# Kernel tuning notes

Hardware: AMD Instinct MI355X
Metric: run time of the kernel (lower is better)

## Reference

```python
import jax, jax.numpy as jnp
import numpy as np

B, S, D, H = 2, 2048, 1024, 16
DH = D // H
MASK_FACTOR = -10000.0
EPS = 1e-6


def setup_inputs() -> dict:
    key = jax.random.key(0)
    ks = jax.random.split(key, 12)
    sc = 1.0 / np.sqrt(D)
    inp = {
        'query': jax.random.normal(ks[0], (B, S, D), jnp.float32),
        'key':   jax.random.normal(ks[1], (B, S, D), jnp.float32),
        'value': jax.random.normal(ks[2], (B, S, D), jnp.float32),
        # mask: 1.0 = masked position (causal), shape (B, 1, Sq, Sk)
        'mask': jnp.broadcast_to(
            (1.0 - jnp.tril(jnp.ones((S, S), jnp.float32)))[None, None], (B, 1, S, S)
        ),
        'wq_w': jax.random.normal(ks[3], (D, D), jnp.float32) * sc,
        'wq_b': jnp.zeros((D,), jnp.float32),
        'wk_w': jax.random.normal(ks[4], (D, D), jnp.float32) * sc,
        'wk_b': jnp.zeros((D,), jnp.float32),
        'wv_w': jax.random.normal(ks[5], (D, D), jnp.float32) * sc,
        'wv_b': jnp.zeros((D,), jnp.float32),
        'wo_w': jax.random.normal(ks[6], (D, D), jnp.float32) * sc,
        'wo_b': jnp.zeros((D,), jnp.float32),
        'ln_g': jnp.ones((D,), jnp.float32),
        'ln_b': jnp.zeros((D,), jnp.float32),
    }
    return inp


def _split_heads(x):
    # (B, S, D) -> (B, H, S, DH)
    b, s, _ = x.shape
    return x.reshape(b, s, H, DH).transpose(0, 2, 1, 3)


def _layer_norm(x, g, b):
    mu = jnp.mean(x, axis=-1, keepdims=True)
    var = jnp.mean(jnp.square(x - mu), axis=-1, keepdims=True)
    return (x - mu) * jax.lax.rsqrt(var + EPS) * g + b


def reference(query, key, value, mask, wq_w, wq_b, wk_w, wk_b, wv_w, wv_b,
              wo_w, wo_b, ln_g, ln_b):
    q = _split_heads(query @ wq_w + wq_b)
    k = _split_heads(key @ wk_w + wk_b)
    v = _split_heads(value @ wv_w + wv_b)

    logits = jnp.einsum('bhqd,bhkd->bhqk', q, k) / jnp.sqrt(jnp.float32(DH))
    logits = logits * (1.0 - mask) + mask * MASK_FACTOR
    attn = jax.nn.softmax(logits, axis=-1)  # (B, H, Sq, Sk)

    ctx = jnp.einsum('bhqk,bhkd->bhqd', attn, v)
    ctx = ctx.transpose(0, 2, 1, 3).reshape(query.shape[0], -1, D)

    out = ctx @ wo_w + wo_b
    out = out + query  # residual
    out = _layer_norm(out, ln_g, ln_b)
    return out, attn
```

## Files before the change

### kernel.cpp

```cpp
#include <hip/hip_runtime.h>

#define B_ 2
#define S_ 2048
#define D_ 1024
#define H_ 16
#define DH_ 64
#define EPS_ 1e-6f

typedef short bf16x8 __attribute__((ext_vector_type(8)));
typedef float f32x4  __attribute__((ext_vector_type(4)));

__device__ __forceinline__ ushort f2bf(float x) {
    uint u = __float_as_uint(x);
    return (ushort)((u + 0x7fffu + ((u >> 16) & 1u)) >> 16);
}
__device__ __forceinline__ float bf2f(ushort h) {
    return __uint_as_float(((uint)h) << 16);
}
__device__ __forceinline__ void split_bf(float x, ushort& hi, ushort& lo) {
    hi = f2bf(x);
    lo = f2bf(x - bf2f(hi));
}

__global__ __launch_bounds__(256) void prep_weights_kernel(
    const float* __restrict__ w0, const float* __restrict__ w1,
    const float* __restrict__ w2, const float* __restrict__ w3,
    ushort* __restrict__ Wth, ushort* __restrict__ Wtl)
{
    const int wi = blockIdx.z;
    const float* W = (wi == 0) ? w0 : (wi == 1) ? w1 : (wi == 2) ? w2 : w3;
    ushort* th = Wth + (size_t)wi * D_ * D_;
    ushort* tl = Wtl + (size_t)wi * D_ * D_;
    const int k0 = blockIdx.x * 32, n0 = blockIdx.y * 32;
    const int tid = threadIdx.x;
    __shared__ float t[32][33];
#pragma unroll
    for (int l = 0; l < 4; ++l) {
        int idx = tid + l * 256;
        int kk = idx >> 5, nn = idx & 31;
        t[kk][nn] = W[(size_t)(k0 + kk) * D_ + n0 + nn];
    }
    __syncthreads();
#pragma unroll
    for (int l = 0; l < 4; ++l) {
        int idx = tid + l * 256;
        int nn = idx >> 5, kk = idx & 31;
        ushort h, lo;
        split_bf(t[kk][nn], h, lo);
        th[(size_t)(n0 + nn) * D_ + k0 + kk] = h;
        tl[(size_t)(n0 + nn) * D_ + k0 + kk] = lo;
    }
}

template <int MODE>
__device__ __forceinline__ void gemm_mfma_body(
    const float* __restrict__ A, const ushort* __restrict__ Bh,
    const ushort* __restrict__ Bl, const float* __restrict__ bias,
    const float* __restrict__ residual, float* __restrict__ Cf,
    ushort* __restrict__ Ch, ushort* __restrict__ Cl,
    int M, int N, int K, int bx, int by)
{
    __shared__ ushort Ah[128][40];
    __shared__ ushort Al[128][40];

    const int tid = threadIdx.x;
    const int lane = tid & 63, w = tid >> 6;
    const int l15 = lane & 15, l4 = lane >> 4;
    const int row0 = by * 128, col0 = bx * 128;
    const int wm = (w >> 1) * 64, wn = (w & 1) * 64;

    const f32x4 zf = {0.f, 0.f, 0.f, 0.f};
    f32x4 acc[4][4];
#pragma unroll
    for (int i = 0; i < 4; ++i)
#pragma unroll
        for (int j = 0; j < 4; ++j) acc[i][j] = zf;

    for (int k0 = 0; k0 < K; k0 += 32) {
#pragma unroll
        for (int l = 0; l < 4; ++l) {
            int idx = tid + l * 256;
            int r = idx >> 3, c4 = (idx & 7) * 4;
            const float4 a = *(const float4*)&A[(size_t)(row0 + r) * K + k0 + c4];
            ushort h0, h1, h2, h3, q0, q1, q2, q3;
            split_bf(a.x, h0, q0); split_bf(a.y, h1, q1);
            split_bf(a.z, h2, q2); split_bf(a.w, h3, q3);
            *(ushort4*)&Ah[r][c4] = make_ushort4(h0, h1, h2, h3);
            *(ushort4*)&Al[r][c4] = make_ushort4(q0, q1, q2, q3);
        }
        bf16x8 bh_[4], bl_[4];
#pragma unroll
        for (int j = 0; j < 4; ++j) {
            const size_t bo = (size_t)(col0 + wn + j * 16 + l15) * K + k0 + l4 * 8;
            bh_[j] = *(const bf16x8*)&Bh[bo];
            bl_[j] = *(const bf16x8*)&Bl[bo];
        }
        __syncthreads();
        bf16x8 ah_[4], al_[4];
#pragma unroll
        for (int i = 0; i < 4; ++i) {
            ah_[i] = *(const bf16x8*)&Ah[wm + i * 16 + l15][l4 * 8];
            al_[i] = *(const bf16x8*)&Al[wm + i * 16 + l15][l4 * 8];
        }
#pragma unroll
        for (int i = 0; i < 4; ++i)
#pragma unroll
            for (int j = 0; j < 4; ++j) {
                acc[i][j] = __builtin_amdgcn_mfma_f32_16x16x32_bf16(
                    ah_[i], bh_[j], acc[i][j], 0, 0, 0);
                acc[i][j] = __builtin_amdgcn_mfma_f32_16x16x32_bf16(
                    ah_[i], bl_[j], acc[i][j], 0, 0, 0);
                acc[i][j] = __builtin_amdgcn_mfma_f32_16x16x32_bf16(
                    al_[i], bh_[j], acc[i][j], 0, 0, 0);
            }
        __syncthreads();
    }

#pragma unroll
    for (int i = 0; i < 4; ++i) {
#pragma unroll
        for (int j = 0; j < 4; ++j) {
            const int col = col0 + wn + j * 16 + l15;
            const float bb = bias[col];
            const int mbase = row0 + wm + i * 16 + l4 * 4;
            if (MODE == 0) {
#pragma unroll
                for (int e = 0; e < 4; ++e) {
                    const int m = mbase + e;
                    float v = acc[i][j][e] + bb;
                    if (residual) v += residual[(size_t)m * N + col];
                    Cf[(size_t)m * N + col] = v;
                }
            } else if (MODE == 1) {
#pragma unroll
                for (int e = 0; e < 4; ++e) {
                    const int m = mbase + e;
                    ushort h, lo;
                    split_bf(acc[i][j][e] + bb, h, lo);
                    Ch[(size_t)m * N + col] = h;
                    Cl[(size_t)m * N + col] = lo;
                }
            } else {
                const int bb_ = mbase / S_;
                const int s0 = mbase - bb_ * S_;
                const int hh = col >> 6, dh = col & 63;
                ushort hv[4], lv[4];
#pragma unroll
                for (int e = 0; e < 4; ++e)
                    split_bf(acc[i][j][e] + bb, hv[e], lv[e]);
                const size_t ofs =
                    (((size_t)bb_ * H_ + hh) * DH_ + dh) * S_ + s0;
                *(ushort4*)&Ch[ofs] = make_ushort4(hv[0], hv[1], hv[2], hv[3]);
                *(ushort4*)&Cl[ofs] = make_ushort4(lv[0], lv[1], lv[2], lv[3]);
            }
        }
    }
}

__global__ __launch_bounds__(256) void gemm_qkv_mfma(
    const float* __restrict__ q, const float* __restrict__ k,
    const float* __restrict__ v,
    const ushort* __restrict__ Wth, const ushort* __restrict__ Wtl,
    const float* __restrict__ bq, const float* __restrict__ bk,
    const float* __restrict__ bv,
    ushort* __restrict__ Qh, ushort* __restrict__ Ql,
    ushort* __restrict__ Kh, ushort* __restrict__ Kl,
    ushort* __restrict__ Vth, ushort* __restrict__ Vtl)
{
    const int z = blockIdx.z;
    const size_t wofs = (size_t)z * D_ * D_;
    if (z == 0)
        gemm_mfma_body<1>(q, Wth, Wtl, bq, nullptr, nullptr, Qh, Ql,
                          B_ * S_, D_, D_, blockIdx.x, blockIdx.y);
    else if (z == 1)
        gemm_mfma_body<1>(k, Wth + wofs, Wtl + wofs, bk, nullptr, nullptr,
                          Kh, Kl, B_ * S_, D_, D_, blockIdx.x, blockIdx.y);
    else
        gemm_mfma_body<2>(v, Wth + wofs, Wtl + wofs, bv, nullptr, nullptr,
                          Vth, Vtl, B_ * S_, D_, D_, blockIdx.x, blockIdx.y);
}

__global__ __launch_bounds__(256) void gemm_out_mfma(
    const float* __restrict__ ctx, const ushort* __restrict__ Wth,
    const ushort* __restrict__ Wtl, const float* __restrict__ bias,
    const float* __restrict__ residual, float* __restrict__ pre)
{
    gemm_mfma_body<0>(ctx, Wth, Wtl, bias, residual, pre, nullptr, nullptr,
                      B_ * S_, D_, D_, blockIdx.x, blockIdx.y);
}

#define RS_ 2056

__global__ __launch_bounds__(1024) void qksm_kernel(
    const ushort* __restrict__ Qh, const ushort* __restrict__ Ql,
    const ushort* __restrict__ Kh, const ushort* __restrict__ Kl,
    float* __restrict__ attn)
{
    extern __shared__ float S_lds[];
    const int bh = blockIdx.x;
    const int strip = blockIdx.y;
    const int b = bh >> 4, h = bh & 15;
    const int s0 = strip * 16;
    const int tid = threadIdx.x;
    const int w = tid >> 6, lane = tid & 63;
    const int l15 = lane & 15, l4 = lane >> 4;
    const int lenmax = s0 + 16;

    const size_t qbase = ((size_t)b * S_ + s0 + l15) * D_ + h * DH_ + l4 * 8;
    const bf16x8 ah0 = *(const bf16x8*)&Qh[qbase];
    const bf16x8 ah1 = *(const bf16x8*)&Qh[qbase + 32];
    const bf16x8 al0 = *(const bf16x8*)&Ql[qbase];
    const bf16x8 al1 = *(const bf16x8*)&Ql[qbase + 32];

    for (int jf = 0; jf < 8; ++jf) {
        const int k0 = w * 128 + jf * 16;
        if (k0 >= lenmax) break;
        const size_t kb = ((size_t)b * S_ + k0 + l15) * D_ + h * DH_ + l4 * 8;
        const bf16x8 bh0 = *(const bf16x8*)&Kh[kb];
        const bf16x8 bh1 = *(const bf16x8*)&Kh[kb + 32];
        const bf16x8 bl0 = *(const bf16x8*)&Kl[kb];
        const bf16x8 bl1 = *(const bf16x8*)&Kl[kb + 32];
        f32x4 acc = {0.f, 0.f, 0.f, 0.f};
        acc = __builtin_amdgcn_mfma_f32_16x16x32_bf16(ah0, bh0, acc, 0, 0, 0);
        acc = __builtin_amdgcn_mfma_f32_16x16x32_bf16(ah0, bl0, acc, 0, 0, 0);
        acc = __builtin_amdgcn_mfma_f32_16x16x32_bf16(al0, bh0, acc, 0, 0, 0);
        acc = __builtin_amdgcn_mfma_f32_16x16x32_bf16(ah1, bh1, acc, 0, 0, 0);
        acc = __builtin_amdgcn_mfma_f32_16x16x32_bf16(ah1, bl1, acc, 0, 0, 0);
        acc = __builtin_amdgcn_mfma_f32_16x16x32_bf16(al1, bh1, acc, 0, 0, 0);
#pragma unroll
        for (int e = 0; e < 4; ++e)
            S_lds[(l4 * 4 + e) * RS_ + k0 + l15] = acc[e] * 0.125f;
    }
    __syncthreads();

    const int qi = s0 + w;
    const int len = qi + 1;
    const int len4 = (len + 3) >> 2;
    float* Srow = &S_lds[w * RS_];

    float lmax = -INFINITY;
    for (int j4 = lane; j4 < len4; j4 += 64) {
        float4 v = *(const float4*)&Srow[j4 * 4];
        const int j = j4 * 4;
        if (j + 1 >= len) v.y = -INFINITY;
        if (j + 2 >= len) v.z = -INFINITY;
        if (j + 3 >= len) v.w = -INFINITY;
        lmax = fmaxf(fmaxf(lmax, fmaxf(v.x, v.y)), fmaxf(v.z, v.w));
    }
#pragma unroll
    for (int o = 32; o > 0; o >>= 1) lmax = fmaxf(lmax, __shfl_xor(lmax, o));
    const float m = lmax;

    float lsum = 0.f;
    for (int j4 = lane; j4 < len4; j4 += 64) {
        float4 v = *(float4*)&Srow[j4 * 4];
        const int j = j4 * 4;
        float4 e;
        e.x = (j     < len) ? __expf(v.x - m) : 0.f;
        e.y = (j + 1 < len) ? __expf(v.y - m) : 0.f;
        e.z = (j + 2 < len) ? __expf(v.z - m) : 0.f;
        e.w = (j + 3 < len) ? __expf(v.w - m) : 0.f;
        *(float4*)&Srow[j4 * 4] = e;
        lsum += e.x + e.y + e.z + e.w;
    }
#pragma unroll
    for (int o = 32; o > 0; o >>= 1) lsum += __shfl_xor(lsum, o);
    const float inv = 1.f / lsum;

    float4* out4 = (float4*)(attn + ((size_t)bh * S_ + qi) * S_);
    for (int j4 = lane; j4 < S_ / 4; j4 += 64) {
        float4 o = {0.f, 0.f, 0.f, 0.f};
        if (j4 < len4) {
            const float4 e = *(const float4*)&Srow[j4 * 4];
            o.x = e.x * inv; o.y = e.y * inv; o.z = e.z * inv; o.w = e.w * inv;
        }
        out4[j4] = o;
    }
}

__global__ __launch_bounds__(256) void pv_mfma_kernel(
    const float* __restrict__ P, const ushort* __restrict__ Vth,
    const ushort* __restrict__ Vtl, float* __restrict__ ctx)
{
    const int tq = blockIdx.x, bh = blockIdx.y, sp = blockIdx.z;
    if (sp > tq) return;
    const int b = bh >> 4, h = bh & 15;
    const int tid = threadIdx.x;
    const int lane = tid & 63, w = tid >> 6;
    const int l15 = lane & 15, l4 = lane >> 4;
    const int wm = w * 64;

    __shared__ ushort Ph[256][40];
    __shared__ ushort Pl[256][40];

    const float* Arow = P + ((size_t)bh * S_ + (size_t)tq * 256) * S_;
    const size_t vbase = ((size_t)b * H_ + h) * (size_t)DH_ * S_;

    const f32x4 zf = {0.f, 0.f, 0.f, 0.f};
    f32x4 acc[4][4];
#pragma unroll
    for (int i = 0; i < 4; ++i)
#pragma unroll
        for (int j = 0; j < 4; ++j) acc[i][j] = zf;

    const int kb = sp * 256;
    for (int k0 = kb; k0 < kb + 256; k0 += 32) {
#pragma unroll
        for (int l = 0; l < 8; ++l) {
            int idx = tid + l * 256;
            int r = idx >> 3, c4 = (idx & 7) * 4;
            const float4 a = *(const float4*)&Arow[(size_t)r * S_ + k0 + c4];
            ushort h0, h1, h2, h3, q0, q1, q2, q3;
            split_bf(a.x, h0, q0); split_bf(a.y, h1, q1);
            split_bf(a.z, h2, q2); split_bf(a.w, h3, q3);
            *(ushort4*)&Ph[r][c4] = make_ushort4(h0, h1, h2, h3);
            *(ushort4*)&Pl[r][c4] = make_ushort4(q0, q1, q2, q3);
        }
        bf16x8 bh_[4], bl_[4];
#pragma unroll
        for (int j = 0; j < 4; ++j) {
            const size_t vo = vbase + (size_t)(j * 16 + l15) * S_ + k0 + l4 * 8;
            bh_[j] = *(const bf16x8*)&Vth[vo];
            bl_[j] = *(const bf16x8*)&Vtl[vo];
        }
        __syncthreads();
        bf16x8 ah_[4], al_[4];
#pragma unroll
        for (int i = 0; i < 4; ++i) {
            ah_[i] = *(const bf16x8*)&Ph[wm + i * 16 + l15][l4 * 8];
            al_[i] = *(const bf16x8*)&Pl[wm + i * 16 + l15][l4 * 8];
        }
#pragma unroll
        for (int i = 0; i < 4; ++i)
#pragma unroll
            for (int j = 0; j < 4; ++j) {
                acc[i][j] = __builtin_amdgcn_mfma_f32_16x16x32_bf16(
                    ah_[i], bh_[j], acc[i][j], 0, 0, 0);
                acc[i][j] = __builtin_amdgcn_mfma_f32_16x16x32_bf16(
                    ah_[i], bl_[j], acc[i][j], 0, 0, 0);
                acc[i][j] = __builtin_amdgcn_mfma_f32_16x16x32_bf16(
                    al_[i], bh_[j], acc[i][j], 0, 0, 0);
            }
        __syncthreads();
    }

    float* C = ctx + ((size_t)b * S_ + (size_t)tq * 256 + wm) * D_ + h * DH_;
#pragma unroll
    for (int i = 0; i < 4; ++i)
#pragma unroll
        for (int j = 0; j < 4; ++j) {
            const int col = j * 16 + l15;
#pragma unroll
            for (int e = 0; e < 4; ++e) {
                const int m = i * 16 + l4 * 4 + e;
                atomicAdd(&C[(size_t)m * D_ + col], acc[i][j][e]);
            }
        }
}

__global__ __launch_bounds__(256) void ln_kernel(
    const float* __restrict__ X, const float* __restrict__ gamma,
    const float* __restrict__ beta, float* __restrict__ out)
{
    const int row = blockIdx.x;
    const int tid = threadIdx.x;
    const float* x = X + (size_t)row * D_;
    __shared__ float red[256];

    float s = 0.f;
    for (int i = tid; i < D_; i += 256) s += x[i];
    red[tid] = s;
    __syncthreads();
    for (int t = 128; t > 0; t >>= 1) {
        if (tid < t) red[tid] += red[tid + t];
        __syncthreads();
    }
    const float mu = red[0] * (1.f / D_);
    __syncthreads();

    float v = 0.f;
    for (int i = tid; i < D_; i += 256) {
        float t = x[i] - mu;
        v += t * t;
    }
    red[tid] = v;
    __syncthreads();
    for (int t = 128; t > 0; t >>= 1) {
        if (tid < t) red[tid] += red[tid + t];
        __syncthreads();
    }
    const float r = rsqrtf(red[0] * (1.f / D_) + EPS_);

    for (int i = tid; i < D_; i += 256) {
        float o = (x[i] - mu) * r * gamma[i] + beta[i];
        out[(size_t)row * D_ + i] = o;
    }
}

extern "C" void kernel_launch(void* const* d_in, const int* in_sizes, int n_in,
                              void* d_out, int out_size, void* d_ws, size_t ws_size,
                              hipStream_t stream)
{
    const float* query = (const float*)d_in[0];
    const float* key   = (const float*)d_in[1];
    const float* value = (const float*)d_in[2];
    const float* wq_w = (const float*)d_in[4];
    const float* wq_b = (const float*)d_in[5];
    const float* wk_w = (const float*)d_in[6];
    const float* wk_b = (const float*)d_in[7];
    const float* wv_w = (const float*)d_in[8];
    const float* wv_b = (const float*)d_in[9];
    const float* wo_w = (const float*)d_in[10];
    const float* wo_b = (const float*)d_in[11];
    const float* ln_g = (const float*)d_in[12];
    const float* ln_b = (const float*)d_in[13];

    float* out_f  = (float*)d_out;
    float* attn_f = out_f + (size_t)B_ * S_ * D_;

    const size_t NELEM = (size_t)B_ * S_ * D_;
    const size_t WELEM = (size_t)4 * D_ * D_;
    char* p = (char*)d_ws;
    ushort* Wth = (ushort*)p; p += WELEM * 2;
    ushort* Wtl = (ushort*)p; p += WELEM * 2;
    ushort* Qh  = (ushort*)p; p += NELEM * 2;
    ushort* Ql  = (ushort*)p; p += NELEM * 2;
    ushort* Kh  = (ushort*)p; p += NELEM * 2;
    ushort* Kl  = (ushort*)p; p += NELEM * 2;
    ushort* Vth = (ushort*)p; p += NELEM * 2;
    ushort* Vtl = (ushort*)p; p += NELEM * 2;
    float*  ctx = (float*)p;  p += NELEM * 4;
    float*  pre = (float*)p;  p += NELEM * 4;

    hipLaunchKernelGGL(prep_weights_kernel, dim3(D_ / 32, D_ / 32, 4), dim3(256),
                       0, stream, wq_w, wk_w, wv_w, wo_w, Wth, Wtl);

    hipLaunchKernelGGL(gemm_qkv_mfma, dim3(D_ / 128, (B_ * S_) / 128, 3),
                       dim3(256), 0, stream,
                       query, key, value, Wth, Wtl, wq_b, wk_b, wv_b,
                       Qh, Ql, Kh, Kl, Vth, Vtl);

    hipMemsetAsync(ctx, 0, NELEM * sizeof(float), stream);

    hipLaunchKernelGGL(qksm_kernel, dim3(B_ * H_, S_ / 16), dim3(1024),
                       16 * RS_ * sizeof(float), stream,
                       Qh, Ql, Kh, Kl, attn_f);

    hipLaunchKernelGGL(pv_mfma_kernel, dim3(S_ / 256, B_ * H_, S_ / 256),
                       dim3(256), 0, stream, attn_f, Vth, Vtl, ctx);

    hipLaunchKernelGGL(gemm_out_mfma, dim3(D_ / 128, (B_ * S_) / 128),
                       dim3(256), 0, stream,
                       ctx, Wth + (size_t)3 * D_ * D_, Wtl + (size_t)3 * D_ * D_,
                       wo_b, query, pre);

    hipLaunchKernelGGL(ln_kernel, dim3(B_ * S_), dim3(256), 0, stream,
                       pre, ln_g, ln_b, out_f);
}
```

Baseline: 1.147 ms.

## Fuse P·V into the QK-softmax kernel using on-chip unnormalized probabilities

The separate PV kernel, which re-read the full fp32 attention matrix from global memory and accumulated ctx with atomics, is removed. The softmax kernel now computes P·V directly from the exponentials held in LDS, using split-bf16 MFMA. Each wave handles a 128-key slice, partial sums are reduced through LDS, and the result is scaled by the per-row inverse sum. This drops the ctx memset, the large attention re-read and the atomics. In exchange the softmax kernel gains more work and extra barriers, and the exponentials are zero-filled up to a 32 boundary so the tail does not read stale LDS.

```diff
diff --git a/kernel.cpp b/kernel.cpp
--- a/kernel.cpp
+++ b/kernel.cpp
@@ -189,14 +189,16 @@
                       B_ * S_, D_, D_, blockIdx.x, blockIdx.y);
 }
 
-#define RS_ 2056
-
-__global__ __launch_bounds__(1024) void qksm_kernel(
+#define RS_ 2052
+
+__global__ __launch_bounds__(1024) void qksm_pv_kernel(
     const ushort* __restrict__ Qh, const ushort* __restrict__ Ql,
     const ushort* __restrict__ Kh, const ushort* __restrict__ Kl,
-    float* __restrict__ attn)
+    const ushort* __restrict__ Vth, const ushort* __restrict__ Vtl,
+    float* __restrict__ attn, float* __restrict__ ctx)
 {
     extern __shared__ float S_lds[];
+    __shared__ float redinv[16];
     const int bh = blockIdx.x;
     const int strip = blockIdx.y;
     const int b = bh >> 4, h = bh & 15;
@@ -236,6 +238,7 @@
     const int qi = s0 + w;
     const int len = qi + 1;
     const int len4 = (len + 3) >> 2;
+    const int Zf4 = ((lenmax + 31) & ~31) >> 2;
     float* Srow = &S_lds[w * RS_];
 
     float lmax = -INFINITY;
@@ -252,7 +255,7 @@
     const float m = lmax;
 
     float lsum = 0.f;
-    for (int j4 = lane; j4 < len4; j4 += 64) {
+    for (int j4 = lane; j4 < Zf4; j4 += 64) {
         float4 v = *(float4*)&Srow[j4 * 4];
         const int j = j4 * 4;
         float4 e;
@@ -266,96 +269,69 @@
 #pragma unroll
     for (int o = 32; o > 0; o >>= 1) lsum += __shfl_xor(lsum, o);
     const float inv = 1.f / lsum;
-
+    if (lane == 0) redinv[w] = inv;
+
+    const int Lmax4 = lenmax >> 2;
     float4* out4 = (float4*)(attn + ((size_t)bh * S_ + qi) * S_);
     for (int j4 = lane; j4 < S_ / 4; j4 += 64) {
         float4 o = {0.f, 0.f, 0.f, 0.f};
-        if (j4 < len4) {
+        if (j4 < Lmax4) {
             const float4 e = *(const float4*)&Srow[j4 * 4];
             o.x = e.x * inv; o.y = e.y * inv; o.z = e.z * inv; o.w = e.w * inv;
         }
         out4[j4] = o;
     }
-}
-
-__global__ __launch_bounds__(256) void pv_mfma_kernel(
-    const float* __restrict__ P, const ushort* __restrict__ Vth,
-    const ushort* __restrict__ Vtl, float* __restrict__ ctx)
-{
-    const int tq = blockIdx.x, bh = blockIdx.y, sp = blockIdx.z;
-    if (sp > tq) return;
-    const int b = bh >> 4, h = bh & 15;
-    const int tid = threadIdx.x;
-    const int lane = tid & 63, w = tid >> 6;
-    const int l15 = lane & 15, l4 = lane >> 4;
-    const int wm = w * 64;
-
-    __shared__ ushort Ph[256][40];
-    __shared__ ushort Pl[256][40];
-
-    const float* Arow = P + ((size_t)bh * S_ + (size_t)tq * 256) * S_;
-    const size_t vbase = ((size_t)b * H_ + h) * (size_t)DH_ * S_;
-
+    __syncthreads();
+
+    const int nact = strip / 8 + 1;
     const f32x4 zf = {0.f, 0.f, 0.f, 0.f};
-    f32x4 acc[4][4];
-#pragma unroll
-    for (int i = 0; i < 4; ++i)
-#pragma unroll
-        for (int j = 0; j < 4; ++j) acc[i][j] = zf;
-
-    const int kb = sp * 256;
-    for (int k0 = kb; k0 < kb + 256; k0 += 32) {
-#pragma unroll
-        for (int l = 0; l < 8; ++l) {
-            int idx = tid + l * 256;
-            int r = idx >> 3, c4 = (idx & 7) * 4;
-            const float4 a = *(const float4*)&Arow[(size_t)r * S_ + k0 + c4];
-            ushort h0, h1, h2, h3, q0, q1, q2, q3;
-            split_bf(a.x, h0, q0); split_bf(a.y, h1, q1);
-            split_bf(a.z, h2, q2); split_bf(a.w, h3, q3);
-            *(ushort4*)&Ph[r][c4] = make_ushort4(h0, h1, h2, h3);
-            *(ushort4*)&Pl[r][c4] = make_ushort4(q0, q1, q2, q3);
-        }
-        bf16x8 bh_[4], bl_[4];
-#pragma unroll
-        for (int j = 0; j < 4; ++j) {
-            const size_t vo = vbase + (size_t)(j * 16 + l15) * S_ + k0 + l4 * 8;
-            bh_[j] = *(const bf16x8*)&Vth[vo];
-            bl_[j] = *(const bf16x8*)&Vtl[vo];
-        }
-        __syncthreads();
-        bf16x8 ah_[4], al_[4];
-#pragma unroll
-        for (int i = 0; i < 4; ++i) {
-            ah_[i] = *(const bf16x8*)&Ph[wm + i * 16 + l15][l4 * 8];
-            al_[i] = *(const bf16x8*)&Pl[wm + i * 16 + l15][l4 * 8];
-        }
-#pragma unroll
-        for (int i = 0; i < 4; ++i)
+    f32x4 pacc[4] = {zf, zf, zf, zf};
+    if (w < nact) {
+        const size_t vbase = ((size_t)b * H_ + h) * (size_t)DH_ * S_;
+        for (int c = 0; c < 4; ++c) {
+            const int k0 = w * 128 + c * 32;
+            if (k0 >= lenmax) break;
+            const float* prow = &S_lds[l15 * RS_ + k0 + l4 * 8];
+            const float4 p0 = *(const float4*)&prow[0];
+            const float4 p1 = *(const float4*)&prow[4];
+            bf16x8 pah, pal;
+            {
+                ushort hh, ll;
+                split_bf(p0.x, hh, ll); pah[0] = (short)hh; pal[0] = (short)ll;
+                split_bf(p0.y, hh, ll); pah[1] = (short)hh; pal[1] = (short)ll;
+                split_bf(p0.z, hh, ll); pah[2] = (short)hh; pal[2] = (short)ll;
+                split_bf(p0.w, hh, ll); pah[3] = (short)hh; pal[3] = (short)ll;
+                split_bf(p1.x, hh, ll); pah[4] = (short)hh; pal[4] = (short)ll;
+                split_bf(p1.y, hh, ll); pah[5] = (short)hh; pal[5] = (short)ll;
+                split_bf(p1.z, hh, ll); pah[6] = (short)hh; pal[6] = (short)ll;
+                split_bf(p1.w, hh, ll); pah[7] = (short)hh; pal[7] = (short)ll;
+            }
 #pragma unroll
             for (int j = 0; j < 4; ++j) {
-                acc[i][j] = __builtin_amdgcn_mfma_f32_16x16x32_bf16(
-                    ah_[i], bh_[j], acc[i][j], 0, 0, 0);
-                acc[i][j] = __builtin_amdgcn_mfma_f32_16x16x32_bf16(
-                    ah_[i], bl_[j], acc[i][j], 0, 0, 0);
-                acc[i][j] = __builtin_amdgcn_mfma_f32_16x16x32_bf16(
-                    al_[i], bh_[j], acc[i][j], 0, 0, 0);
+                const size_t vo = vbase + (size_t)(j * 16 + l15) * S_ + k0 + l4 * 8;
+                const bf16x8 vh = *(const bf16x8*)&Vth[vo];
+                const bf16x8 vl = *(const bf16x8*)&Vtl[vo];
+                pacc[j] = __builtin_amdgcn_mfma_f32_16x16x32_bf16(
+                    pah, vh, pacc[j], 0, 0, 0);
+                pacc[j] = __builtin_amdgcn_mfma_f32_16x16x32_bf16(
+                    pah, vl, pacc[j], 0, 0, 0);
+                pacc[j] = __builtin_amdgcn_mfma_f32_16x16x32_bf16(
+                    pal, vh, pacc[j], 0, 0, 0);
             }
-        __syncthreads();
-    }
-
-    float* C = ctx + ((size_t)b * S_ + (size_t)tq * 256 + wm) * D_ + h * DH_;
-#pragma unroll
-    for (int i = 0; i < 4; ++i)
-#pragma unroll
-        for (int j = 0; j < 4; ++j) {
-            const int col = j * 16 + l15;
-#pragma unroll
-            for (int e = 0; e < 4; ++e) {
-                const int m = i * 16 + l4 * 4 + e;
-                atomicAdd(&C[(size_t)m * D_ + col], acc[i][j][e]);
-            }
-        }
+        }
+#pragma unroll
+        for (int j = 0; j < 4; ++j)
+#pragma unroll
+            for (int e = 0; e < 4; ++e)
+                S_lds[(l4 * 4 + e) * RS_ + w * 128 + j * 16 + l15] = pacc[j][e];
+    }
+    __syncthreads();
+
+    const int r5 = tid >> 6, dh5 = tid & 63;
+    float s5 = 0.f;
+    for (int ww = 0; ww < nact; ++ww)
+        s5 += S_lds[r5 * RS_ + ww * 128 + dh5];
+    ctx[((size_t)b * S_ + s0 + r5) * D_ + h * DH_ + dh5] = s5 * redinv[r5];
 }
 
 __global__ __launch_bounds__(256) void ln_kernel(
@@ -440,14 +416,9 @@
                        query, key, value, Wth, Wtl, wq_b, wk_b, wv_b,
                        Qh, Ql, Kh, Kl, Vth, Vtl);
 
-    hipMemsetAsync(ctx, 0, NELEM * sizeof(float), stream);
-
-    hipLaunchKernelGGL(qksm_kernel, dim3(B_ * H_, S_ / 16), dim3(1024),
+    hipLaunchKernelGGL(qksm_pv_kernel, dim3(B_ * H_, S_ / 16), dim3(1024),
                        16 * RS_ * sizeof(float), stream,
-                       Qh, Ql, Kh, Kl, attn_f);
-
-    hipLaunchKernelGGL(pv_mfma_kernel, dim3(S_ / 256, B_ * H_, S_ / 256),
-                       dim3(256), 0, stream, attn_f, Vth, Vtl, ctx);
+                       Qh, Ql, Kh, Kl, Vth, Vtl, attn_f, ctx);
 
     hipLaunchKernelGGL(gemm_out_mfma, dim3(D_ / 128, (B_ * S_) / 128),
                        dim3(256), 0, stream,
```

Measured after the change: 1.114 ms. 1.03x faster.
